# Performance work log

Measured on AMD Instinct MI355X. Metric: run time of the kernel, lower is better.

The kernel has to match this reference:

```python
import jax, jax.numpy as jnp
import numpy as np


def _lstm_layer(x, W_ih, W_hh, b):
    # x: [B, T, D_in]; W_ih: [4H, D_in]; W_hh: [4H, H]; b: [4H]
    H = W_hh.shape[1]
    # Precompute input-to-hidden GEMM for all timesteps (batched, efficient).
    xg = jnp.einsum('bti,gi->btg', x, W_ih) + b  # [B, T, 4H]
    B = x.shape[0]
    h0 = jnp.zeros((B, H), dtype=x.dtype)
    c0 = jnp.zeros((B, H), dtype=x.dtype)

    def step(carry, xg_t):
        h, c = carry
        g = xg_t + h @ W_hh.T                     # [B, 4H]
        i, f, gg, o = jnp.split(g, 4, axis=-1)    # torch LSTMCell gate order
        i = jax.nn.sigmoid(i)
        f = jax.nn.sigmoid(f)
        gg = jnp.tanh(gg)
        o = jax.nn.sigmoid(o)
        c = f * c + i * gg
        h = o * jnp.tanh(c)
        return (h, c), h

    (h_last, c_last), hs = jax.lax.scan(step, (h0, c0), jnp.swapaxes(xg, 0, 1))
    return jnp.swapaxes(hs, 0, 1), h_last, c_last  # [B,T,H], [B,H], [B,H]


def setup_inputs() -> dict:
    key = jax.random.key(0)
    ks = jax.random.split(key, 6)
    B, T, D, H = 64, 2048, 256, 256
    s = 0.05  # small init scale for numerical stability over 2048 steps
    return {
        'x': jax.random.normal(ks[0], (B, T, D), dtype=jnp.float32),
        'W_ih0': jax.random.normal(ks[1], (4 * H, D), dtype=jnp.float32) * s,
        'W_hh0': jax.random.normal(ks[2], (4 * H, H), dtype=jnp.float32) * s,
        'b0': jnp.zeros((4 * H,), dtype=jnp.float32),
        'W_ih1': jax.random.normal(ks[3], (4 * H, H), dtype=jnp.float32) * s,
        'W_hh1': jax.random.normal(ks[4], (4 * H, H), dtype=jnp.float32) * s,
        'b1': jnp.zeros((4 * H,), dtype=jnp.float32),
    }


def reference(x, W_ih0, W_hh0, b0, W_ih1, W_hh1, b1):
    # 2-layer unidirectional LSTM, matching RNNBase(mode='LSTM') forward:
    # returns (h_seq_of_last_layer [B,T,H], (h_last, c_last) of last layer)
    h1, _, _ = _lstm_layer(x, W_ih0, W_hh0, b0)
    h2, h_last, c_last = _lstm_layer(h1, W_ih1, W_hh1, b1)
    return h2, h_last, c_last
```

## Files before the change

kernel.cpp:

```cpp
#include <hip/hip_runtime.h>
#include <hip/hip_bf16.h>


typedef unsigned short u16;
typedef unsigned int   u32;

typedef __attribute__((ext_vector_type(8))) _Float16       half8;
typedef __attribute__((ext_vector_type(2))) _Float16       half2_t;
typedef __attribute__((ext_vector_type(8))) unsigned short ushort8;
typedef __attribute__((ext_vector_type(4))) float          f32x4;

#define B_  64
#define T_  2048
#define D_  256
#define H_  256
#define G_  1024

#define NRG 46
#define NLD 18
static_assert(NRG + NLD == 64, "k-half coverage");

__device__ __forceinline__ u16 f2h(float f) {
    union { _Float16 h; u16 b; } v; v.h = (_Float16)f; return v.b;
}
__device__ __forceinline__ float dot2(u32 w, u32 hv, float acc) {
#if __has_builtin(__builtin_amdgcn_fdot2)
    union { u32 u; half2_t h; } a, b;
    a.u = w; b.u = hv;
    return __builtin_amdgcn_fdot2(a.h, b.h, acc, false);
#else
    union { u32 u; _Float16 h[2]; } a, b;
    a.u = w; b.u = hv;
    acc += (float)a.h[0] * (float)b.h[0];
    acc += (float)a.h[1] * (float)b.h[1];
    return acc;
#endif
}
__device__ __forceinline__ float pl32_red(float x) {
    u32 u = __float_as_uint(x), v = u;
    asm("v_permlane32_swap_b32 %0, %1" : "+v"(u), "+v"(v));
    return __uint_as_float(u) + __uint_as_float(v);
}
__device__ __forceinline__ float sigm(float x) {
    return 1.0f / (1.0f + __expf(-x));
}
__device__ __forceinline__ float tanh_(float x) {
    float e = __expf(-2.0f * fabsf(x));
    float r = (1.0f - e) / (1.0f + e);
    return x < 0.0f ? -r : r;
}

__global__ __launch_bounds__(256) void pack_whh(
    const float* __restrict__ W0, const float* __restrict__ W1,
    uint4* __restrict__ P0, uint4* __restrict__ P1)
{
    const int k2 = blockIdx.x;
    const int j  = threadIdx.x;
    const float* W = blockIdx.y ? W1 : W0;
    uint4*       P = blockIdx.y ? P1 : P0;
    uint4 v;
    u32* vp = &v.x;
#pragma unroll
    for (int g = 0; g < 4; ++g) {
        float2 w = *(const float2*)(W + (size_t)(g * 256 + j) * 256 + 2 * k2);
        vp[g] = (u32)f2h(w.x) | ((u32)f2h(w.y) << 16);
    }
    P[(size_t)k2 * 256 + j] = v;
}

__global__ __launch_bounds__(256) void pack_wih(
    const float* __restrict__ W0, const float* __restrict__ W1,
    u16* __restrict__ O0, u16* __restrict__ O1)
{
    const float* W = blockIdx.y ? W1 : W0;
    u16*         O = blockIdx.y ? O1 : O0;
    size_t i = (size_t)blockIdx.x * 256 + threadIdx.x;
    float4 v = ((const float4*)W)[i];
    u32 lo = (u32)f2h(v.x) | ((u32)f2h(v.y) << 16);
    u32 hi = (u32)f2h(v.z) | ((u32)f2h(v.w) << 16);
    uint2 u; u.x = lo; u.y = hi;
    ((uint2*)O)[i] = u;
}

struct GemmJob {
    const void* Av;
    const u16*  Bh;
    u16*        out;
    int tclog2, Tstride, t0, ahalf, active;
};

__global__ __launch_bounds__(256) void gemm_xg2(GemmJob GA, GemmJob GB)
{
    const GemmJob G = blockIdx.y ? GB : GA;
    if (!G.active) return;
    __shared__ __align__(16) u16 As[64][264];
    const int tid    = threadIdx.x;
    const int m0     = blockIdx.x * 64;
    const int tcmask = (1 << G.tclog2) - 1;

    if (G.ahalf) {
        const u16* Ah = (const u16*)G.Av;
#pragma unroll
        for (int it = 0; it < 8; ++it) {
            int idx = it * 256 + tid;
            int row = idx >> 5;
            int c8  = idx & 31;
            int m   = m0 + row;
            size_t grow = (size_t)(m >> G.tclog2) * G.Tstride + G.t0 + (m & tcmask);
            ushort8 v = *(const ushort8*)(Ah + grow * D_ + c8 * 8);
            *(ushort8*)(&As[row][c8 * 8]) = v;
        }
    } else {
        const float* Af = (const float*)G.Av;
#pragma unroll
        for (int it = 0; it < 16; ++it) {
            int idx = it * 256 + tid;
            int row = idx >> 6;
            int c4  = idx & 63;
            int m   = m0 + row;
            size_t grow = (size_t)(m >> G.tclog2) * G.Tstride + G.t0 + (m & tcmask);
            float4 v = *(const float4*)(Af + grow * D_ + c4 * 4);
            uint2 u;
            u.x = (u32)f2h(v.x) | ((u32)f2h(v.y) << 16);
            u.y = (u32)f2h(v.z) | ((u32)f2h(v.w) << 16);
            *(uint2*)(&As[row][c4 * 4]) = u;
        }
    }
    __syncthreads();

    const int l   = tid & 63;
    const int w   = tid >> 6;
    const int rl  = l & 15;
    const int kg  = l >> 4;
    const int rr0 = kg * 4;
    u16* out = G.out;

    for (int nb = 0; nb < 8; ++nb) {
        const int n0 = nb * 128 + w * 32;
        f32x4 zz = {0.f, 0.f, 0.f, 0.f};
        f32x4 acc[4][2];
#pragma unroll
        for (int mi = 0; mi < 4; ++mi)
#pragma unroll
            for (int ni = 0; ni < 2; ++ni) acc[mi][ni] = zz;

#pragma unroll
        for (int ks = 0; ks < 8; ++ks) {
            const int k = ks * 32 + kg * 8;
            half8 a[4], bb[2];
#pragma unroll
            for (int mi = 0; mi < 4; ++mi)
                a[mi] = *(const half8*)(&As[mi * 16 + rl][k]);
#pragma unroll
            for (int ni = 0; ni < 2; ++ni)
                bb[ni] = *(const half8*)(G.Bh + (size_t)(n0 + ni * 16 + rl) * D_ + k);
#pragma unroll
            for (int mi = 0; mi < 4; ++mi)
#pragma unroll
                for (int ni = 0; ni < 2; ++ni)
                    acc[mi][ni] = __builtin_amdgcn_mfma_f32_16x16x32_f16(
                        a[mi], bb[ni], acc[mi][ni], 0, 0, 0);
        }

#pragma unroll
        for (int mi = 0; mi < 4; ++mi)
#pragma unroll
            for (int ni = 0; ni < 2; ++ni) {
                f32x4 d = acc[mi][ni];
                size_t mrow = (size_t)(m0 + mi * 16 + rr0);
                int col = n0 + ni * 16 + rl;
#pragma unroll
                for (int r = 0; r < 4; ++r)
                    out[(mrow + r) * G_ + col] = f2h(d[r]);
            }
    }
}

struct ScanJob {
    const _Float16* xg;
    const uint4*    Wp;
    const float*    bias;
    float*          state;
    void*           h_out;
    float*          hc_last;
    int Tc;
    int toff;
    int TS;
    int houth;
    int first;
};

__global__ __launch_bounds__(512, 2) void lstm_scan2(ScanJob JA, ScanJob JB)
{
    const ScanJob J = (blockIdx.x >= 64) ? JB : JA;
    if (J.Tc == 0) return;
    const int b    = blockIdx.x & 63;
    const int tid  = threadIdx.x;
    const int w    = tid >> 6;
    const int lane = tid & 63;
    const int kh   = lane >> 5;
    const int jl   = lane & 31;
    const int j    = w * 32 + jl;

    __shared__ __align__(16) uint4    wl[NLD][512];
    __shared__ __align__(16) _Float16 hf2[2][256];

    const uint4* wpb = J.Wp + (size_t)(kh * 64) * 256 + j;
    uint4 wr[NRG];
#pragma unroll
    for (int p = 0; p < NRG; ++p)
        wr[p] = wpb[(size_t)p * 256];
#pragma unroll
    for (int p = 0; p < NLD; ++p)
        wl[p][tid] = wpb[(size_t)(NRG + p) * 256];

    const int Tc    = J.Tc;
    const int houth = J.houth;
    float h = 0.f, c = 0.f;
    float bi = 0.f, bf_ = 0.f, bg = 0.f, bo = 0.f;
    const _Float16* xg = J.xg;
    size_t xo = (size_t)b * Tc * G_ + j;
    float nx0 = 0.f, nx1 = 0.f, nx2 = 0.f, nx3 = 0.f;

    if (!J.first) {
        h = J.state[b * H_ + j];
        c = J.state[B_ * H_ + b * H_ + j];
    }
    if (kh == 0) {
        bi  = J.bias[j];
        bf_ = J.bias[256 + j];
        bg  = J.bias[512 + j];
        bo  = J.bias[768 + j];
        hf2[0][j] = (_Float16)h;
        nx0 = (float)xg[xo];       nx1 = (float)xg[xo + 256];
        nx2 = (float)xg[xo + 512]; nx3 = (float)xg[xo + 768];
    }
    float* hof = (float*)J.h_out;
    u16*   hoh = (u16*)J.h_out;
    size_t ho = ((size_t)b * J.TS + J.toff) * H_ + j;
    __syncthreads();

    for (int t = 0; t < Tc; ++t) {
        const int par = t & 1;
        float a0, a1, a2, a3;
        if (kh == 0) {
            a0 = nx0 + bi; a1 = nx1 + bf_; a2 = nx2 + bg; a3 = nx3 + bo;
            if (t + 1 < Tc) xo += G_;
            nx0 = (float)xg[xo];       nx1 = (float)xg[xo + 256];
            nx2 = (float)xg[xo + 512]; nx3 = (float)xg[xo + 768];
        } else {
            a0 = a1 = a2 = a3 = 0.f;
        }

        const uint4* hvp = ((const uint4*)hf2[par]) + kh * 16;
#pragma unroll
        for (int i = 0; i < 16; ++i) {
            uint4 hv4 = hvp[i];
            const u32* hq = &hv4.x;
#pragma unroll
            for (int q = 0; q < 4; ++q) {
                const int p = 4 * i + q;
                uint4 wv;
                if (p < NRG) wv = wr[p];
                else         wv = wl[p - NRG][tid];
                u32 hv = hq[q];
                a0 = dot2(wv.x, hv, a0);
                a1 = dot2(wv.y, hv, a1);
                a2 = dot2(wv.z, hv, a2);
                a3 = dot2(wv.w, hv, a3);
            }
        }

        a0 = pl32_red(a0);
        a1 = pl32_red(a1);
        a2 = pl32_red(a2);
        a3 = pl32_red(a3);

        float i_ = sigm(a0);
        float f_ = sigm(a1);
        float g_ = tanh_(a2);
        float o_ = sigm(a3);
        c = f_ * c + i_ * g_;
        float hn = o_ * tanh_(c);
        h = hn;
        if (kh == 0) {
            hf2[par ^ 1][j] = (_Float16)hn;
            if (houth) hoh[ho] = f2h(hn);
            else       __builtin_nontemporal_store(hn, hof + ho);
            ho += H_;
        }
        __syncthreads();
    }

    if (kh == 0) {
        J.state[b * H_ + j] = h;
        J.state[B_ * H_ + b * H_ + j] = c;
        if (J.hc_last) {
            J.hc_last[b * H_ + j] = h;
            J.hc_last[B_ * H_ + b * H_ + j] = c;
        }
    }
}

extern "C" void kernel_launch(void* const* d_in, const int* in_sizes, int n_in,
                              void* d_out, int out_size, void* d_ws, size_t ws_size,
                              hipStream_t stream)
{
    (void)in_sizes; (void)n_in; (void)out_size;

    const float* x    = (const float*)d_in[0];
    const float* Wih0 = (const float*)d_in[1];
    const float* Whh0 = (const float*)d_in[2];
    const float* b0   = (const float*)d_in[3];
    const float* Wih1 = (const float*)d_in[4];
    const float* Whh1 = (const float*)d_in[5];
    const float* b1   = (const float*)d_in[6];

    float* out   = (float*)d_out;
    float* hlast = out + (size_t)B_ * T_ * H_;

    char* ws = (char*)d_ws;
    const size_t WPB  = (size_t)128 * 256 * 16;
    const size_t WIHB = (size_t)1024 * 256 * 2;
    const size_t STB  = (size_t)2 * B_ * H_ * 4;
    uint4* Wp0    = (uint4*)(ws);
    uint4* Wp1    = (uint4*)(ws + WPB);
    u16*   Wih0h  = (u16*)(ws + 2 * WPB);
    u16*   Wih1h  = (u16*)(ws + 2 * WPB + WIHB);
    float* state0 = (float*)(ws + 2 * WPB + 2 * WIHB);
    float* state1 = (float*)(ws + 2 * WPB + 2 * WIHB + STB);
    const size_t BASE = 2 * WPB + 2 * WIHB + 2 * STB;

    int Tc = 16;
    for (int tc = 256; tc >= 16; tc >>= 1)
        if (BASE + (size_t)tc * 294912 <= ws_size) { Tc = tc; break; }
    const int nch    = T_ / Tc;
    const int tclog2 = 31 - __builtin_clz((unsigned)Tc);
    const size_t H1CB = (size_t)B_ * Tc * H_ * 2;
    const size_t XGB  = (size_t)B_ * Tc * G_ * 2;
    u16*      h1c = (u16*)(ws + BASE);
    _Float16* xgA = (_Float16*)(ws + BASE + H1CB);
    _Float16* xgB = (_Float16*)(ws + BASE + H1CB + XGB);

    pack_whh<<<dim3(128, 2), 256, 0, stream>>>(Whh0, Whh1, Wp0, Wp1);
    pack_wih<<<dim3(256, 2), 256, 0, stream>>>(Wih0, Wih1, Wih0h, Wih1h);

    const int gemmWG = (B_ * Tc) / 64;

    {
        GemmJob GA = {}; GA.active = 1;
        GA.Av = x; GA.Bh = Wih0h; GA.out = (u16*)xgA;
        GA.tclog2 = tclog2; GA.Tstride = T_; GA.t0 = 0; GA.ahalf = 0;
        GemmJob GB = {}; GB.active = 0;
        gemm_xg2<<<dim3(gemmWG, 2), 256, 0, stream>>>(GA, GB);
    }

    for (int s = 0; s <= nch; ++s) {
        ScanJob JA = {}; JA.Tc = 0;
        ScanJob JB = {}; JB.Tc = 0;
        if (s < nch) {
            JA.xg = xgA;  JA.Wp = Wp0;  JA.bias = b0;  JA.state = state0;
            JA.h_out = h1c;  JA.hc_last = nullptr;
            JA.Tc = Tc;  JA.toff = 0;  JA.TS = Tc;  JA.houth = 1;
            JA.first = (s == 0);
        }
        if (s >= 1) {
            int cc = s - 1;
            JB.xg = xgB;  JB.Wp = Wp1;  JB.bias = b1;  JB.state = state1;
            JB.h_out = out;  JB.hc_last = (cc == nch - 1) ? hlast : nullptr;
            JB.Tc = Tc;  JB.toff = cc * Tc;  JB.TS = T_;  JB.houth = 0;
            JB.first = (cc == 0);
        }
        lstm_scan2<<<128, 512, 0, stream>>>(JA, JB);

        GemmJob GA = {}; GA.active = 0;
        GemmJob GB = {}; GB.active = 0;
        if (s + 1 < nch) {
            GA.active = 1; GA.Av = x; GA.Bh = Wih0h; GA.out = (u16*)xgA;
            GA.tclog2 = tclog2; GA.Tstride = T_; GA.t0 = (s + 1) * Tc; GA.ahalf = 0;
        }
        if (s < nch) {
            GB.active = 1; GB.Av = h1c; GB.Bh = Wih1h; GB.out = (u16*)xgB;
            GB.tclog2 = tclog2; GB.Tstride = Tc; GB.t0 = 0; GB.ahalf = 1;
        }
        if (GA.active || GB.active)
            gemm_xg2<<<dim3(gemmWG, 2), 256, 0, stream>>>(GA, GB);
    }
}
```

Measured before the change: 4.754 ms.

## Split K-halves across wave halves with LDS reduction instead of permlane swap

Changes the thread mapping so threads 0-255 and 256-511 each cover half of the K dimension for all 256 hidden units, rather than splitting K within each wave and combining with v_permlane32_swap. The two partial sums are now combined through an LDS float4 buffer, and only half the threads compute the gate nonlinearities. This adds a second __syncthreads per timestep and leaves half the threads idle during the activation phase. The h buffer is single-buffered now that the extra barrier orders reads and writes, in exchange for one less cross-lane permute per gate.

```diff
diff --git a/kernel.cpp b/kernel.cpp
--- a/kernel.cpp
+++ b/kernel.cpp
@@ -18,7 +18,7 @@
 
 #define NRG 46
 #define NLD 18
-static_assert(NRG + NLD == 64, "k-half coverage");
+static_assert(NRG + NLD == 64, "k-split coverage");
 
 __device__ __forceinline__ u16 f2h(float f) {
     union { _Float16 h; u16 b; } v; v.h = (_Float16)f; return v.b;
@@ -35,11 +35,6 @@
     acc += (float)a.h[1] * (float)b.h[1];
     return acc;
 #endif
-}
-__device__ __forceinline__ float pl32_red(float x) {
-    u32 u = __float_as_uint(x), v = u;
-    asm("v_permlane32_swap_b32 %0, %1" : "+v"(u), "+v"(v));
-    return __uint_as_float(u) + __uint_as_float(v);
 }
 __device__ __forceinline__ float sigm(float x) {
     return 1.0f / (1.0f + __expf(-x));
@@ -194,16 +189,14 @@
 {
     const ScanJob J = (blockIdx.x >= 64) ? JB : JA;
     if (J.Tc == 0) return;
-    const int b    = blockIdx.x & 63;
-    const int tid  = threadIdx.x;
-    const int w    = tid >> 6;
-    const int lane = tid & 63;
-    const int kh   = lane >> 5;
-    const int jl   = lane & 31;
-    const int j    = w * 32 + jl;
-
-    __shared__ __align__(16) uint4    wl[NLD][512];
-    __shared__ __align__(16) _Float16 hf2[2][256];
+    const int b   = blockIdx.x & 63;
+    const int tid = threadIdx.x;
+    const int j   = tid & 255;
+    const int kh  = tid >> 8;
+
+    __shared__ __align__(16) uint4  wl[NLD][512];
+    __shared__ __align__(16) u32    hf_p[128];
+    __shared__ __align__(16) float4 red[256];
 
     const uint4* wpb = J.Wp + (size_t)(kh * 64) * 256 + j;
     uint4 wr[NRG];
@@ -214,34 +207,35 @@
     for (int p = 0; p < NLD; ++p)
         wl[p][tid] = wpb[(size_t)(NRG + p) * 256];
 
-    const int Tc    = J.Tc;
+    const int Tc = J.Tc;
     const int houth = J.houth;
     float h = 0.f, c = 0.f;
     float bi = 0.f, bf_ = 0.f, bg = 0.f, bo = 0.f;
     const _Float16* xg = J.xg;
     size_t xo = (size_t)b * Tc * G_ + j;
     float nx0 = 0.f, nx1 = 0.f, nx2 = 0.f, nx3 = 0.f;
-
-    if (!J.first) {
-        h = J.state[b * H_ + j];
-        c = J.state[B_ * H_ + b * H_ + j];
-    }
+    _Float16* hfh = (_Float16*)hf_p;
+
     if (kh == 0) {
+        if (!J.first) {
+            h = J.state[b * H_ + j];
+            c = J.state[B_ * H_ + b * H_ + j];
+        }
         bi  = J.bias[j];
         bf_ = J.bias[256 + j];
         bg  = J.bias[512 + j];
         bo  = J.bias[768 + j];
-        hf2[0][j] = (_Float16)h;
+        hfh[j] = (_Float16)h;
         nx0 = (float)xg[xo];       nx1 = (float)xg[xo + 256];
         nx2 = (float)xg[xo + 512]; nx3 = (float)xg[xo + 768];
     }
+    const uint4* hv4p = ((const uint4*)hf_p) + kh * 16;
     float* hof = (float*)J.h_out;
     u16*   hoh = (u16*)J.h_out;
     size_t ho = ((size_t)b * J.TS + J.toff) * H_ + j;
     __syncthreads();
 
     for (int t = 0; t < Tc; ++t) {
-        const int par = t & 1;
         float a0, a1, a2, a3;
         if (kh == 0) {
             a0 = nx0 + bi; a1 = nx1 + bf_; a2 = nx2 + bg; a3 = nx3 + bo;
@@ -252,10 +246,9 @@
             a0 = a1 = a2 = a3 = 0.f;
         }
 
-        const uint4* hvp = ((const uint4*)hf2[par]) + kh * 16;
 #pragma unroll
         for (int i = 0; i < 16; ++i) {
-            uint4 hv4 = hvp[i];
+            uint4 hv4 = hv4p[i];
             const u32* hq = &hv4.x;
 #pragma unroll
             for (int q = 0; q < 4; ++q) {
@@ -271,20 +264,22 @@
             }
         }
 
-        a0 = pl32_red(a0);
-        a1 = pl32_red(a1);
-        a2 = pl32_red(a2);
-        a3 = pl32_red(a3);
-
-        float i_ = sigm(a0);
-        float f_ = sigm(a1);
-        float g_ = tanh_(a2);
-        float o_ = sigm(a3);
-        c = f_ * c + i_ * g_;
-        float hn = o_ * tanh_(c);
-        h = hn;
+        if (kh == 1) {
+            float4 r4; r4.x = a0; r4.y = a1; r4.z = a2; r4.w = a3;
+            red[j] = r4;
+        }
+        __syncthreads();
         if (kh == 0) {
-            hf2[par ^ 1][j] = (_Float16)hn;
+            float4 r4 = red[j];
+            a0 += r4.x; a1 += r4.y; a2 += r4.z; a3 += r4.w;
+            float i_ = sigm(a0);
+            float f_ = sigm(a1);
+            float g_ = tanh_(a2);
+            float o_ = sigm(a3);
+            c = f_ * c + i_ * g_;
+            float hn = o_ * tanh_(c);
+            h = hn;
+            hfh[j] = (_Float16)hn;
             if (houth) hoh[ho] = f2h(hn);
             else       __builtin_nontemporal_store(hn, hof + ho);
             ho += H_;
```

Result: faster. 3.922 ms (-17.5%).
